# Kernel tuning notes

Measured on AMD Instinct MI355X. Metric: run time of the kernel, lower is better.

The kernel has to match this reference:

```python
import jax, jax.numpy as jnp
import numpy as np

N, E, B = 20000, 320000, 2
IN, HID, HEADS, OUT = 32, 64, 4, 8
N_MP = 2
SLOPE = 0.2  # GATConv default negative_slope


def setup_inputs() -> dict:
    key = jax.random.key(0)
    ks = jax.random.split(key, 10)
    s = 0.1
    return {
        "h": jax.random.normal(ks[0], (B, N, IN), jnp.float32),
        "edge_index": jax.random.randint(ks[1], (2, E), 0, N),
        "W_enc": jax.random.normal(ks[2], (IN, HID), jnp.float32) * s,
        "b_enc": jnp.zeros((HID,), jnp.float32),
        "W_gat": jax.random.normal(ks[3], (HID, HEADS * HID), jnp.float32) * s,
        "a_l": jax.random.normal(ks[4], (HEADS, HID), jnp.float32) * s,
        "a_r": jax.random.normal(ks[5], (HEADS, HID), jnp.float32) * s,
        "b_gat": jnp.zeros((HEADS * HID,), jnp.float32),
        "W_res": jax.random.normal(ks[6], (HID, HID), jnp.float32) * s,
        "b_res": jnp.zeros((HID,), jnp.float32),
        "W_dec": jax.random.normal(ks[7], (HID, OUT), jnp.float32) * s,
        "b_dec": jnp.zeros((OUT,), jnp.float32),
    }


def _gat(x, src, dst, W_gat, a_l, a_r, b_gat):
    # x: [N, B, HID] -> per-head projected features [N, B, HEADS, HID]
    ft = (x @ W_gat).reshape(N, B, HEADS, HID)
    el = jnp.einsum("nbhd,hd->nbh", ft, a_l)  # src attention term
    er = jnp.einsum("nbhd,hd->nbh", ft, a_r)  # dst attention term
    e = el[src] + er[dst]                      # [E, B, HEADS]
    e = jnp.where(e > 0, e, SLOPE * e)         # LeakyReLU
    # segment softmax over incoming edges of each dst node
    m = jax.ops.segment_max(e, dst, num_segments=N)
    e = jnp.exp(e - m[dst])
    z = jax.ops.segment_sum(e, dst, num_segments=N)
    alpha = e / z[dst]                         # [E, B, HEADS]
    msg = alpha[..., None] * ft[src]           # [E, B, HEADS, HID]
    agg = jax.ops.segment_sum(msg, dst, num_segments=N)
    return agg + b_gat.reshape(HEADS, HID)     # [N, B, HEADS, HID]


def reference(h, edge_index, W_enc, b_enc, W_gat, a_l, a_r, b_gat,
              W_res, b_res, W_dec, b_dec):
    src, dst = edge_index[0], edge_index[1]
    x = jnp.transpose(h, (1, 0, 2))            # [N, B, IN]
    x = x @ W_enc + b_enc                      # encoder (dropout in eval = identity)
    for _ in range(N_MP):
        gat_out = _gat(x, src, dst, W_gat, a_l, a_r, b_gat)
        x = jax.nn.elu(gat_out.mean(-2) + x @ W_res + b_res)
    x = x @ W_dec + b_dec
    return jnp.transpose(x, (1, 0, 2))         # [B, N, OUT]
```

## Files before the change

### kernel.cpp

```cpp
#include <hip/hip_runtime.h>
#include <hip/hip_bf16.h>

#define N_NODES 20000
#define N_EDGES 320000
#define BATCH 2
#define IN_DIM 32
#define HID 64
#define HEADS 4
#define OUT_DIM 8
#define ROWS (N_NODES * BATCH)
#define SLOPE 0.2f

typedef __hip_bfloat16 bf16;
typedef short v8s __attribute__((ext_vector_type(8)));
typedef float v4f __attribute__((ext_vector_type(4)));

#define WS_XA       0
#define WS_XB       1280000
#define WS_ELA      2560000
#define WS_ERA      2720000
#define WS_ELB      2880000
#define WS_ERB      3040000
#define WS_DEG      3200000
#define WS_ROWSTART 3220032
#define WS_CUR      3240064
#define WS_CSRC     3260096
#define WS_WGBPK    3580096
#define WS_WRESBPK  3588288
#define WS_WX8PK    3590336
#define WS_WENCBPK  3590848
#define WS_WDECBPK  3591872
#define WS_BGM      3592384
#define WS_END      3592448

__device__ __forceinline__ float us2f(unsigned short u) {
    union { unsigned int i; float f; } z; z.i = ((unsigned int)u) << 16; return z.f;
}
__device__ __forceinline__ unsigned short f2us(float f) {
    bf16 b = __float2bfloat16(f);
    return *(unsigned short*)&b;
}
__device__ __forceinline__ float ld(const void* p, int i, int isbf) {
    if (isbf) return us2f(((const unsigned short*)p)[i]);
    return ((const float*)p)[i];
}
__device__ __forceinline__ float lrexp(float v) {
    v = v > 0.f ? v : SLOPE * v;
    return __expf(fminf(v, 60.f));
}

__device__ __forceinline__ int sniff64(const void* h) {
    const unsigned short* u = (const unsigned short*)h;
    int lane = threadIdx.x & 63;
    unsigned short v = u[2 * lane];
    int ef = (v >> 7) & 0xFF;
    unsigned long long m = __ballot(ef >= 100 && ef <= 150);
    return __popcll(m) >= 48;
}

__global__ __launch_bounds__(256) void k_prep(const void* __restrict__ h,
                                              const void* __restrict__ Wg,
                                              const void* __restrict__ al,
                                              const void* __restrict__ ar,
                                              const void* __restrict__ Wr,
                                              const void* __restrict__ We,
                                              const void* __restrict__ Wd,
                                              const void* __restrict__ bg,
                                              unsigned short* __restrict__ WgBpk,
                                              unsigned short* __restrict__ WresBpk,
                                              unsigned short* __restrict__ Wx8pk,
                                              unsigned short* __restrict__ WencBpk,
                                              unsigned short* __restrict__ WdecBpk,
                                              float* __restrict__ bgm,
                                              int* __restrict__ deg) {
    int t = threadIdx.x, b = blockIdx.x;
    if (b >= 18) {
        int base = (b - 18) * 1024 + t * 4;
#pragma unroll
        for (int i = 0; i < 4; i++)
            if (base + i < 20032) deg[base + i] = 0;
        return;
    }
    const int isbf = sniff64(h);
    if (b < 16) {
#pragma unroll
        for (int q = 0; q < 4; q++) {
            int idx = b * 1024 + q * 256 + t;
            int j = idx & 7, m16 = (idx >> 3) & 15, quad = (idx >> 7) & 3;
            int ks = (idx >> 9) & 1, ct = (idx >> 10) & 3, hh = (idx >> 12) & 3;
            int k = ks * 32 + quad * 8 + j;
            int c = hh * 64 + ct * 16 + m16;
            WgBpk[idx] = f2us(ld(Wg, k * 256 + c, isbf));
        }
    } else if (b == 16) {
#pragma unroll
        for (int q = 0; q < 4; q++) {
            int idx = q * 256 + t;
            int j = idx & 7, m16 = (idx >> 3) & 15, quad = (idx >> 7) & 3;
            int ks = (idx >> 9) & 1;
            int k = ks * 32 + quad * 8 + j;
            float v = 0.f;
            if (m16 < 8) {
                int hh = m16 & 3, lr = m16 >> 2;
                const void* a = lr ? ar : al;
                for (int d = 0; d < 64; d++)
                    v += ld(Wg, k * 256 + hh * 64 + d, isbf) * ld(a, hh * 64 + d, isbf);
            }
            Wx8pk[idx] = f2us(v);
        }
#pragma unroll
        for (int q = 0; q < 8; q++) {
            int idx = q * 256 + t;
            int j = idx & 7, m16 = (idx >> 3) & 15, quad = (idx >> 7) & 3, ct = idx >> 9;
            int k = quad * 8 + j;
            WencBpk[idx] = f2us(ld(We, k * 64 + ct * 16 + m16, isbf));
        }
#pragma unroll
        for (int q = 0; q < 4; q++) {
            int idx = q * 256 + t;
            int j = idx & 7, m16 = (idx >> 3) & 15, quad = (idx >> 7) & 3;
            int ks = (idx >> 9) & 1;
            int k = ks * 32 + quad * 8 + j;
            WdecBpk[idx] = (m16 < 8) ? f2us(ld(Wd, k * 8 + m16, isbf)) : (unsigned short)0;
        }
        if (t < 64) {
            float s = 0.f;
            for (int hh = 0; hh < 4; hh++) s += ld(bg, hh * 64 + t, isbf);
            bgm[t] = 0.25f * s;
        }
    } else {
#pragma unroll
        for (int q = 0; q < 16; q++) {
            int idx = q * 256 + t;
            int j = idx & 7, m16 = (idx >> 3) & 15, quad = (idx >> 7) & 3;
            int ks = (idx >> 9) & 1;
            int k = ks * 32 + quad * 8 + j;
            WresBpk[idx] = f2us(ld(Wr, k * 64 + ((idx >> 10) & 3) * 16 + m16, isbf));
        }
    }
}

__global__ __launch_bounds__(256) void k_hist(const int* __restrict__ dst, int* __restrict__ deg) {
    int e = blockIdx.x * 256 + threadIdx.x;
    if (e < N_EDGES) atomicAdd(&deg[dst[e]], 1);
}

__global__ __launch_bounds__(1024) void k_scan(const int* __restrict__ deg,
                                               int* __restrict__ rowstart,
                                               int* __restrict__ cursor) {
    __shared__ int ssum[1024];
    int t = threadIdx.x;
    int base = t * 20;
    int local[20];
    int s = 0;
#pragma unroll
    for (int i = 0; i < 20; i++) {
        int v = (base + i < N_NODES) ? deg[base + i] : 0;
        local[i] = s;
        s += v;
    }
    ssum[t] = s;
    __syncthreads();
    for (int off = 1; off < 1024; off <<= 1) {
        int v = (t >= off) ? ssum[t - off] : 0;
        __syncthreads();
        if (t >= off) ssum[t] += v;
        __syncthreads();
    }
    int prev = (t == 0) ? 0 : ssum[t - 1];
#pragma unroll
    for (int i = 0; i < 20; i++) {
        if (base + i < N_NODES) {
            int v = prev + local[i];
            rowstart[base + i] = v;
            cursor[base + i] = v;
        }
    }
    if (t == 1023) rowstart[N_NODES] = ssum[1023];
}

__global__ __launch_bounds__(256) void k_scatter(const int* __restrict__ src,
                                                 const int* __restrict__ dst,
                                                 int* __restrict__ cursor,
                                                 int* __restrict__ csrc) {
    int e = blockIdx.x * 256 + threadIdx.x;
    if (e >= N_EDGES) return;
    int pos = atomicAdd(&cursor[dst[e]], 1);
    csrc[pos] = src[e];
}

__global__ __launch_bounds__(256) void k_enc2(const void* __restrict__ h,
                                              const unsigned short* __restrict__ WencBpk,
                                              const void* __restrict__ benc,
                                              const unsigned short* __restrict__ Wx8pk,
                                              unsigned int* __restrict__ xb32,
                                              float* __restrict__ el,
                                              float* __restrict__ er) {
    const int isbf = sniff64(h);
    __shared__ unsigned short sXb[64 * 64];
    int t = threadIdx.x;
    int w = t >> 6, lane = t & 63, quad = lane >> 4, m16 = lane & 15;
    int row0 = blockIdx.x * 64;
    int grow = row0 + w * 16 + m16;
    int n = grow >> 1, b = grow & 1;

    v8s Af;
    size_t hb = (size_t)(b * N_NODES + n) * IN_DIM + quad * 8;
    if (isbf) {
        Af = *(const v8s*)((const unsigned short*)h + hb);
    } else {
        const float4* hp = (const float4*)((const float*)h + hb);
        float4 xa = hp[0], xbv = hp[1];
        Af[0] = (short)f2us(xa.x);  Af[1] = (short)f2us(xa.y);
        Af[2] = (short)f2us(xa.z);  Af[3] = (short)f2us(xa.w);
        Af[4] = (short)f2us(xbv.x); Af[5] = (short)f2us(xbv.y);
        Af[6] = (short)f2us(xbv.z); Af[7] = (short)f2us(xbv.w);
    }

    v4f acc[4];
#pragma unroll
    for (int ct = 0; ct < 4; ct++) {
        v8s Bf = *(const v8s*)(WencBpk + ((ct << 9) | (quad << 7) | (m16 << 3)));
        acc[ct] = __builtin_amdgcn_mfma_f32_16x16x32_bf16(Af, Bf, (v4f)(0.f), 0, 0, 0);
    }

#pragma unroll
    for (int ct = 0; ct < 4; ct++) {
        int col = ct * 16 + m16;
        float bv = ld(benc, col, isbf);
        float vr[4];
        int rloc0 = w * 16 + quad * 4;
#pragma unroll
        for (int r = 0; r < 4; r++) {
            vr[r] = acc[ct][r] + bv;
            sXb[(rloc0 + r) * 64 + col] = f2us(vr[r]);
        }
        int nd0 = (row0 + rloc0) >> 1;
        xb32[(size_t)nd0 * 64 + col] =
            (unsigned int)f2us(vr[0]) | ((unsigned int)f2us(vr[1]) << 16);
        xb32[(size_t)(nd0 + 1) * 64 + col] =
            (unsigned int)f2us(vr[2]) | ((unsigned int)f2us(vr[3]) << 16);
    }
    __syncthreads();
    v4f e8 = (v4f)(0.f);
#pragma unroll
    for (int ks = 0; ks < 2; ks++) {
        v8s Af2 = *(const v8s*)(sXb + (w * 16 + m16) * 64 + ks * 32 + quad * 8);
        v8s Bf = *(const v8s*)(Wx8pk + (((ks * 4 + quad) << 7) + (m16 << 3)));
        e8 = __builtin_amdgcn_mfma_f32_16x16x32_bf16(Af2, Bf, e8, 0, 0, 0);
    }
    if (m16 < 8) {
#pragma unroll
        for (int r = 0; r < 4; r++) {
            int gr = row0 + w * 16 + quad * 4 + r;
            float v = e8[r];
            if (m16 < 4) el[gr * 4 + m16] = v;
            else         er[gr * 4 + (m16 - 4)] = v;
        }
    }
}

__global__ __launch_bounds__(256) void k_round(const int* __restrict__ rowstart,
                                               const int* __restrict__ csrc,
                                               const float* __restrict__ el_in,
                                               const float* __restrict__ er_in,
                                               const unsigned int* __restrict__ x_in,
                                               const unsigned short* __restrict__ WgBpk,
                                               const unsigned short* __restrict__ WresBpk,
                                               const unsigned short* __restrict__ Wx8pk,
                                               const unsigned short* __restrict__ WdecBpk,
                                               const void* __restrict__ h,
                                               const void* __restrict__ br,
                                               const void* __restrict__ bd,
                                               const float* __restrict__ bgm,
                                               unsigned int* __restrict__ x_out,
                                               float* __restrict__ el_out,
                                               float* __restrict__ er_out,
                                               void* __restrict__ out,
                                               int emit) {
    const int isbf = sniff64(h);
    __shared__ unsigned short sAgg[4 * 16 * 64];
    __shared__ unsigned short sXb[16 * 64];
    int t = threadIdx.x;
    int w = t >> 6, lane = t & 63, quad = lane >> 4, m16 = lane & 15;
    int i8 = m16 & 15 & 7;

    int nA = blockIdx.x * 8 + w * 2;
    int begA = rowstart[nA], endA = rowstart[nA + 1], endB = rowstart[nA + 2];
    int begB = endA;
    int rowNode = (m16 < 8) ? nA : (nA + 1);
    float erv = er_in[rowNode * 8 + i8];
    int beg = (quad < 2) ? begA : begB;
    int end = (quad < 2) ? endA : endB;
    int off = ((quad & 1) << 3);
    int active = ((m16 < 8) == (quad < 2));
    int itA = (endA - begA + 15) >> 4;
    int itB = (endB - begB + 15) >> 4;
    int itmax = itA > itB ? itA : itB;

    v4f accB0[4], accB1[4], accW;
#pragma unroll
    for (int tl = 0; tl < 4; tl++) { accB0[tl] = (v4f)(0.f); accB1[tl] = (v4f)(0.f); }
    accW = (v4f)(0.f);
    v8s Bones;
#pragma unroll
    for (int j = 0; j < 8; j++) Bones[j] = (short)0x3F80;

    for (int it = 0; it < itmax; ++it) {
        int p0 = beg + it * 16 + off;
        int s[8];
#pragma unroll
        for (int j = 0; j < 8; j++) {
            int idx = p0 + j;
            s[j] = csrc[idx < end ? idx : 0];
        }
        v8s Af;
#pragma unroll
        for (int j = 0; j < 8; j++) {
            float wv = 0.f;
            if (active && (p0 + j < end))
                wv = lrexp(el_in[s[j] * 8 + i8] + erv);
            Af[j] = (short)f2us(wv);
        }
        accW = __builtin_amdgcn_mfma_f32_16x16x32_bf16(Af, Bones, accW, 0, 0, 0);
#pragma unroll
        for (int tl = 0; tl < 4; tl++) {
            v8s B0, B1;
#pragma unroll
            for (int j = 0; j < 8; j++) {
                unsigned int q = x_in[(size_t)s[j] * 64 + tl * 16 + m16];
                B0[j] = (short)(q & 0xffffu);
                B1[j] = (short)(q >> 16);
            }
            accB0[tl] = __builtin_amdgcn_mfma_f32_16x16x32_bf16(Af, B0, accB0[tl], 0, 0, 0);
            accB1[tl] = __builtin_amdgcn_mfma_f32_16x16x32_bf16(Af, B1, accB1[tl], 0, 0, 0);
        }
    }

    {
        int row16 = w * 4 + quad;
        int swz = (row16 & 7) << 3;
#pragma unroll
        for (int tl = 0; tl < 4; tl++) {
#pragma unroll
            for (int r = 0; r < 4; r++) {
                float wss = accW[r];
                float mine = (quad & 1) ? accB1[tl][r] : accB0[tl][r];
                float v = (wss > 0.f) ? mine / (4.f * wss) : 0.f;
                int col = tl * 16 + m16;
                sAgg[((r * 16 + row16) << 6) | (col ^ swz)] = f2us(v);
            }
        }
    }
    __syncthreads();

    int grow0 = blockIdx.x * 16;
    int grow = grow0 + m16;
    int nd = grow >> 1;
    unsigned sh = (grow & 1) * 16;
    int ct = w;

    v4f acc = (v4f)(0.f);
#pragma unroll
    for (int hh = 0; hh < 4; hh++) {
#pragma unroll
        for (int ks = 0; ks < 2; ks++) {
            int si = ((hh * 16 + m16) << 6) | ((ks * 32 + quad * 8) ^ ((m16 & 7) << 3));
            v8s Af = *(const v8s*)(sAgg + si);
            v8s Bf = *(const v8s*)(WgBpk + ((hh << 12) | (ct << 10) | (ks << 9) | (quad << 7) | (m16 << 3)));
            acc = __builtin_amdgcn_mfma_f32_16x16x32_bf16(Af, Bf, acc, 0, 0, 0);
        }
    }
#pragma unroll
    for (int ks = 0; ks < 2; ks++) {
        const uint4* xp = (const uint4*)(x_in + (size_t)nd * 64 + ks * 32 + quad * 8);
        uint4 qa = xp[0], qb = xp[1];
        v8s Af;
        Af[0] = (short)((qa.x >> sh) & 0xffffu);
        Af[1] = (short)((qa.y >> sh) & 0xffffu);
        Af[2] = (short)((qa.z >> sh) & 0xffffu);
        Af[3] = (short)((qa.w >> sh) & 0xffffu);
        Af[4] = (short)((qb.x >> sh) & 0xffffu);
        Af[5] = (short)((qb.y >> sh) & 0xffffu);
        Af[6] = (short)((qb.z >> sh) & 0xffffu);
        Af[7] = (short)((qb.w >> sh) & 0xffffu);
        v8s Bf = *(const v8s*)(WresBpk + ((ct << 10) | (ks << 9) | (quad << 7) | (m16 << 3)));
        acc = __builtin_amdgcn_mfma_f32_16x16x32_bf16(Af, Bf, acc, 0, 0, 0);
    }

    {
        int col = ct * 16 + m16;
        float bv = ld(br, col, isbf) + bgm[col];
        float vr[4];
#pragma unroll
        for (int r = 0; r < 4; r++) {
            float v = acc[r] + bv;
            v = v > 0.f ? v : expm1f(v);
            vr[r] = v;
            sXb[(quad * 4 + r) * 64 + col] = f2us(v);
        }
        if (emit) {
            int nd0 = (grow0 + quad * 4) >> 1;
            x_out[(size_t)nd0 * 64 + col] =
                (unsigned int)f2us(vr[0]) | ((unsigned int)f2us(vr[1]) << 16);
            x_out[(size_t)(nd0 + 1) * 64 + col] =
                (unsigned int)f2us(vr[2]) | ((unsigned int)f2us(vr[3]) << 16);
        }
    }
    __syncthreads();

    if (w == 0) {
        if (emit) {
            v4f e8 = (v4f)(0.f);
#pragma unroll
            for (int ks = 0; ks < 2; ks++) {
                v8s Af = *(const v8s*)(sXb + m16 * 64 + ks * 32 + quad * 8);
                v8s Bf = *(const v8s*)(Wx8pk + (((ks * 4 + quad) << 7) + (m16 << 3)));
                e8 = __builtin_amdgcn_mfma_f32_16x16x32_bf16(Af, Bf, e8, 0, 0, 0);
            }
            if (m16 < 8) {
#pragma unroll
                for (int r = 0; r < 4; r++) {
                    int gr = grow0 + quad * 4 + r;
                    float v = e8[r];
                    if (m16 < 4) el_out[gr * 4 + m16] = v;
                    else         er_out[gr * 4 + (m16 - 4)] = v;
                }
            }
        } else {
            v4f o8 = (v4f)(0.f);
#pragma unroll
            for (int ks = 0; ks < 2; ks++) {
                v8s Af = *(const v8s*)(sXb + m16 * 64 + ks * 32 + quad * 8);
                v8s Bf = *(const v8s*)(WdecBpk + ((ks << 9) | (quad << 7) | (m16 << 3)));
                o8 = __builtin_amdgcn_mfma_f32_16x16x32_bf16(Af, Bf, o8, 0, 0, 0);
            }
            if (m16 < 8) {
                float bvd = ld(bd, m16, isbf);
#pragma unroll
                for (int r = 0; r < 4; r++) {
                    int gr = grow0 + quad * 4 + r;
                    int nn = gr >> 1, bb = gr & 1;
                    size_t oi = (size_t)(bb * N_NODES + nn) * OUT_DIM + m16;
                    float v = o8[r] + bvd;
                    if (isbf) ((unsigned short*)out)[oi] = f2us(v);
                    else      ((float*)out)[oi] = v;
                }
            }
        }
    }
}

extern "C" void kernel_launch(void* const* d_in, const int* in_sizes, int n_in,
                              void* d_out, int out_size, void* d_ws, size_t ws_size,
                              hipStream_t stream) {
    const void* h     = d_in[0];
    const int*  ei    = (const int*)d_in[1];
    const void* W_enc = d_in[2];
    const void* b_enc = d_in[3];
    const void* W_gat = d_in[4];
    const void* a_l   = d_in[5];
    const void* a_r   = d_in[6];
    const void* b_gat = d_in[7];
    const void* W_res = d_in[8];
    const void* b_res = d_in[9];
    const void* W_dec = d_in[10];
    const void* b_dec = d_in[11];

    float* ws = (float*)d_ws;
    unsigned int* xA = (unsigned int*)(ws + WS_XA);
    unsigned int* xB = (unsigned int*)(ws + WS_XB);
    float* elA      = ws + WS_ELA;
    float* erA      = ws + WS_ERA;
    float* elB      = ws + WS_ELB;
    float* erB      = ws + WS_ERB;
    int*   deg      = (int*)(ws + WS_DEG);
    int*   rowstart = (int*)(ws + WS_ROWSTART);
    int*   cursor   = (int*)(ws + WS_CUR);
    int*   csrc     = (int*)(ws + WS_CSRC);
    unsigned short* WgBpk   = (unsigned short*)(ws + WS_WGBPK);
    unsigned short* WresBpk = (unsigned short*)(ws + WS_WRESBPK);
    unsigned short* Wx8pk   = (unsigned short*)(ws + WS_WX8PK);
    unsigned short* WencBpk = (unsigned short*)(ws + WS_WENCBPK);
    unsigned short* WdecBpk = (unsigned short*)(ws + WS_WDECBPK);
    float* bgm      = ws + WS_BGM;

    const int* src = ei;
    const int* dst = ei + N_EDGES;

    k_prep<<<38, 256, 0, stream>>>(h, W_gat, a_l, a_r, W_res, W_enc, W_dec, b_gat,
                                   WgBpk, WresBpk, Wx8pk, WencBpk, WdecBpk, bgm, deg);
    k_hist<<<(N_EDGES + 255) / 256, 256, 0, stream>>>(dst, deg);
    k_scan<<<1, 1024, 0, stream>>>(deg, rowstart, cursor);
    k_scatter<<<(N_EDGES + 255) / 256, 256, 0, stream>>>(src, dst, cursor, csrc);

    k_enc2<<<ROWS / 64, 256, 0, stream>>>(h, WencBpk, b_enc, Wx8pk, xA, elA, erA);

    k_round<<<N_NODES / 8, 256, 0, stream>>>(rowstart, csrc, elA, erA, xA,
                                             WgBpk, WresBpk, Wx8pk, WdecBpk,
                                             h, b_res, b_dec, bgm,
                                             xB, elB, erB, d_out, 1);
    k_round<<<N_NODES / 8, 256, 0, stream>>>(rowstart, csrc, elB, erB, xB,
                                             WgBpk, WresBpk, Wx8pk, WdecBpk,
                                             h, b_res, b_dec, bgm,
                                             xA, elA, erA, d_out, 0);
}
```

Measured before the change: 238.6 us.

## Fuse prep, histogram and scan into one kernel; merge scatter with encoder

Replaces the separate prep, global-atomic histogram, single-block scan, scatter and encoder launches with two kernels. k_front has 18 blocks pack weights while 4 blocks each own a 5000-node destination range: each counts degrees in a shared-memory histogram, counts edges below its range for an offset, and scans locally. k_scatter_enc runs the CSR scatter and the encoder in one launch. This removes launch overhead and global atomics on the degree array, but each CSR block now reads all 320k dst indices.

```diff
diff --git a/kernel.cpp b/kernel.cpp
--- a/kernel.cpp
+++ b/kernel.cpp
@@ -21,7 +21,6 @@
 #define WS_ERA      2720000
 #define WS_ELB      2880000
 #define WS_ERB      3040000
-#define WS_DEG      3200000
 #define WS_ROWSTART 3220032
 #define WS_CUR      3240064
 #define WS_CSRC     3260096
@@ -58,30 +57,22 @@
     return __popcll(m) >= 48;
 }
 
-__global__ __launch_bounds__(256) void k_prep(const void* __restrict__ h,
-                                              const void* __restrict__ Wg,
-                                              const void* __restrict__ al,
-                                              const void* __restrict__ ar,
-                                              const void* __restrict__ Wr,
-                                              const void* __restrict__ We,
-                                              const void* __restrict__ Wd,
-                                              const void* __restrict__ bg,
-                                              unsigned short* __restrict__ WgBpk,
-                                              unsigned short* __restrict__ WresBpk,
-                                              unsigned short* __restrict__ Wx8pk,
-                                              unsigned short* __restrict__ WencBpk,
-                                              unsigned short* __restrict__ WdecBpk,
-                                              float* __restrict__ bgm,
-                                              int* __restrict__ deg) {
-    int t = threadIdx.x, b = blockIdx.x;
-    if (b >= 18) {
-        int base = (b - 18) * 1024 + t * 4;
-#pragma unroll
-        for (int i = 0; i < 4; i++)
-            if (base + i < 20032) deg[base + i] = 0;
-        return;
-    }
-    const int isbf = sniff64(h);
+
+__device__ __forceinline__ void prep_body(int b, int isbf,
+                                          const void* __restrict__ Wg,
+                                          const void* __restrict__ al,
+                                          const void* __restrict__ ar,
+                                          const void* __restrict__ Wr,
+                                          const void* __restrict__ We,
+                                          const void* __restrict__ Wd,
+                                          const void* __restrict__ bg,
+                                          unsigned short* __restrict__ WgBpk,
+                                          unsigned short* __restrict__ WresBpk,
+                                          unsigned short* __restrict__ Wx8pk,
+                                          unsigned short* __restrict__ WencBpk,
+                                          unsigned short* __restrict__ WdecBpk,
+                                          float* __restrict__ bgm) {
+    int t = threadIdx.x;
     if (b < 16) {
 #pragma unroll
         for (int q = 0; q < 4; q++) {
@@ -140,67 +131,18 @@
     }
 }
 
-__global__ __launch_bounds__(256) void k_hist(const int* __restrict__ dst, int* __restrict__ deg) {
-    int e = blockIdx.x * 256 + threadIdx.x;
-    if (e < N_EDGES) atomicAdd(&deg[dst[e]], 1);
-}
-
-__global__ __launch_bounds__(1024) void k_scan(const int* __restrict__ deg,
-                                               int* __restrict__ rowstart,
-                                               int* __restrict__ cursor) {
-    __shared__ int ssum[1024];
-    int t = threadIdx.x;
-    int base = t * 20;
-    int local[20];
-    int s = 0;
-#pragma unroll
-    for (int i = 0; i < 20; i++) {
-        int v = (base + i < N_NODES) ? deg[base + i] : 0;
-        local[i] = s;
-        s += v;
-    }
-    ssum[t] = s;
-    __syncthreads();
-    for (int off = 1; off < 1024; off <<= 1) {
-        int v = (t >= off) ? ssum[t - off] : 0;
-        __syncthreads();
-        if (t >= off) ssum[t] += v;
-        __syncthreads();
-    }
-    int prev = (t == 0) ? 0 : ssum[t - 1];
-#pragma unroll
-    for (int i = 0; i < 20; i++) {
-        if (base + i < N_NODES) {
-            int v = prev + local[i];
-            rowstart[base + i] = v;
-            cursor[base + i] = v;
-        }
-    }
-    if (t == 1023) rowstart[N_NODES] = ssum[1023];
-}
-
-__global__ __launch_bounds__(256) void k_scatter(const int* __restrict__ src,
-                                                 const int* __restrict__ dst,
-                                                 int* __restrict__ cursor,
-                                                 int* __restrict__ csrc) {
-    int e = blockIdx.x * 256 + threadIdx.x;
-    if (e >= N_EDGES) return;
-    int pos = atomicAdd(&cursor[dst[e]], 1);
-    csrc[pos] = src[e];
-}
-
-__global__ __launch_bounds__(256) void k_enc2(const void* __restrict__ h,
-                                              const unsigned short* __restrict__ WencBpk,
-                                              const void* __restrict__ benc,
-                                              const unsigned short* __restrict__ Wx8pk,
-                                              unsigned int* __restrict__ xb32,
-                                              float* __restrict__ el,
-                                              float* __restrict__ er) {
-    const int isbf = sniff64(h);
-    __shared__ unsigned short sXb[64 * 64];
+__device__ __forceinline__ void enc_unit(int u, int isbf,
+                                         const void* __restrict__ h,
+                                         const unsigned short* __restrict__ WencBpk,
+                                         const void* __restrict__ benc,
+                                         const unsigned short* __restrict__ Wx8pk,
+                                         unsigned int* __restrict__ xb32,
+                                         float* __restrict__ el,
+                                         float* __restrict__ er,
+                                         unsigned short* __restrict__ sXb) {
     int t = threadIdx.x;
     int w = t >> 6, lane = t & 63, quad = lane >> 4, m16 = lane & 15;
-    int row0 = blockIdx.x * 64;
+    int row0 = u * 64;
     int grow = row0 + w * 16 + m16;
     int n = grow >> 1, b = grow & 1;
 
@@ -258,6 +200,307 @@
             else         er[gr * 4 + (m16 - 4)] = v;
         }
     }
+}
+
+__device__ __forceinline__ void round_unit(int u, int isbf,
+                                           const int* __restrict__ rowstart,
+                                           const int* __restrict__ csrc,
+                                           const float* __restrict__ el_in,
+                                           const float* __restrict__ er_in,
+                                           const unsigned int* __restrict__ x_in,
+                                           const unsigned short* __restrict__ WgBpk,
+                                           const unsigned short* __restrict__ WresBpk,
+                                           const unsigned short* __restrict__ Wx8pk,
+                                           const unsigned short* __restrict__ WdecBpk,
+                                           const void* __restrict__ br,
+                                           const void* __restrict__ bd,
+                                           const float* __restrict__ bgm,
+                                           unsigned int* __restrict__ x_out,
+                                           float* __restrict__ el_out,
+                                           float* __restrict__ er_out,
+                                           void* __restrict__ out,
+                                           int emit,
+                                           unsigned short* __restrict__ sAgg,
+                                           unsigned short* __restrict__ sXb) {
+    int t = threadIdx.x;
+    int w = t >> 6, lane = t & 63, quad = lane >> 4, m16 = lane & 15;
+    int i8 = m16 & 7;
+
+    int nA = u * 8 + w * 2;
+    int begA = rowstart[nA], endA = rowstart[nA + 1], endB = rowstart[nA + 2];
+    int begB = endA;
+    int rowNode = (m16 < 8) ? nA : (nA + 1);
+    float erv = er_in[rowNode * 8 + i8];
+    int beg = (quad < 2) ? begA : begB;
+    int end = (quad < 2) ? endA : endB;
+    int off = ((quad & 1) << 3);
+    int active = ((m16 < 8) == (quad < 2));
+    int itA = (endA - begA + 15) >> 4;
+    int itB = (endB - begB + 15) >> 4;
+    int itmax = itA > itB ? itA : itB;
+
+    v4f accB0[4], accB1[4], accW;
+#pragma unroll
+    for (int tl = 0; tl < 4; tl++) { accB0[tl] = (v4f)(0.f); accB1[tl] = (v4f)(0.f); }
+    accW = (v4f)(0.f);
+    v8s Bones;
+#pragma unroll
+    for (int j = 0; j < 8; j++) Bones[j] = (short)0x3F80;
+
+    for (int it = 0; it < itmax; ++it) {
+        int p0 = beg + it * 16 + off;
+        int s[8];
+#pragma unroll
+        for (int j = 0; j < 8; j++) {
+            int idx = p0 + j;
+            s[j] = csrc[idx < end ? idx : 0];
+        }
+        v8s Af;
+#pragma unroll
+        for (int j = 0; j < 8; j++) {
+            float wv = 0.f;
+            if (active && (p0 + j < end))
+                wv = lrexp(el_in[s[j] * 8 + i8] + erv);
+            Af[j] = (short)f2us(wv);
+        }
+        accW = __builtin_amdgcn_mfma_f32_16x16x32_bf16(Af, Bones, accW, 0, 0, 0);
+#pragma unroll
+        for (int tl = 0; tl < 4; tl++) {
+            v8s B0, B1;
+#pragma unroll
+            for (int j = 0; j < 8; j++) {
+                unsigned int q = x_in[(size_t)s[j] * 64 + tl * 16 + m16];
+                B0[j] = (short)(q & 0xffffu);
+                B1[j] = (short)(q >> 16);
+            }
+            accB0[tl] = __builtin_amdgcn_mfma_f32_16x16x32_bf16(Af, B0, accB0[tl], 0, 0, 0);
+            accB1[tl] = __builtin_amdgcn_mfma_f32_16x16x32_bf16(Af, B1, accB1[tl], 0, 0, 0);
+        }
+    }
+
+    {
+        int row16 = w * 4 + quad;
+        int swz = (row16 & 7) << 3;
+#pragma unroll
+        for (int tl = 0; tl < 4; tl++) {
+#pragma unroll
+            for (int r = 0; r < 4; r++) {
+                float wss = accW[r];
+                float mine = (quad & 1) ? accB1[tl][r] : accB0[tl][r];
+                float v = (wss > 0.f) ? mine / (4.f * wss) : 0.f;
+                int col = tl * 16 + m16;
+                sAgg[((r * 16 + row16) << 6) | (col ^ swz)] = f2us(v);
+            }
+        }
+    }
+    __syncthreads();
+
+    int grow0 = u * 16;
+    int grow = grow0 + m16;
+    int nd = grow >> 1;
+    unsigned sh = (grow & 1) * 16;
+    int ct = w;
+
+    v4f acc = (v4f)(0.f);
+#pragma unroll
+    for (int hh = 0; hh < 4; hh++) {
+#pragma unroll
+        for (int ks = 0; ks < 2; ks++) {
+            int si = ((hh * 16 + m16) << 6) | ((ks * 32 + quad * 8) ^ ((m16 & 7) << 3));
+            v8s Af = *(const v8s*)(sAgg + si);
+            v8s Bf = *(const v8s*)(WgBpk + ((hh << 12) | (ct << 10) | (ks << 9) | (quad << 7) | (m16 << 3)));
+            acc = __builtin_amdgcn_mfma_f32_16x16x32_bf16(Af, Bf, acc, 0, 0, 0);
+        }
+    }
+#pragma unroll
+    for (int ks = 0; ks < 2; ks++) {
+        const uint4* xp = (const uint4*)(x_in + (size_t)nd * 64 + ks * 32 + quad * 8);
+        uint4 qa = xp[0], qb = xp[1];
+        v8s Af;
+        Af[0] = (short)((qa.x >> sh) & 0xffffu);
+        Af[1] = (short)((qa.y >> sh) & 0xffffu);
+        Af[2] = (short)((qa.z >> sh) & 0xffffu);
+        Af[3] = (short)((qa.w >> sh) & 0xffffu);
+        Af[4] = (short)((qb.x >> sh) & 0xffffu);
+        Af[5] = (short)((qb.y >> sh) & 0xffffu);
+        Af[6] = (short)((qb.z >> sh) & 0xffffu);
+        Af[7] = (short)((qb.w >> sh) & 0xffffu);
+        v8s Bf = *(const v8s*)(WresBpk + ((ct << 10) | (ks << 9) | (quad << 7) | (m16 << 3)));
+        acc = __builtin_amdgcn_mfma_f32_16x16x32_bf16(Af, Bf, acc, 0, 0, 0);
+    }
+
+    {
+        int col = ct * 16 + m16;
+        float bv = ld(br, col, isbf) + bgm[col];
+        float vr[4];
+#pragma unroll
+        for (int r = 0; r < 4; r++) {
+            float v = acc[r] + bv;
+            v = v > 0.f ? v : expm1f(v);
+            vr[r] = v;
+            sXb[(quad * 4 + r) * 64 + col] = f2us(v);
+        }
+        if (emit) {
+            int nd0 = (grow0 + quad * 4) >> 1;
+            x_out[(size_t)nd0 * 64 + col] =
+                (unsigned int)f2us(vr[0]) | ((unsigned int)f2us(vr[1]) << 16);
+            x_out[(size_t)(nd0 + 1) * 64 + col] =
+                (unsigned int)f2us(vr[2]) | ((unsigned int)f2us(vr[3]) << 16);
+        }
+    }
+    __syncthreads();
+
+    if (w == 0) {
+        if (emit) {
+            v4f e8 = (v4f)(0.f);
+#pragma unroll
+            for (int ks = 0; ks < 2; ks++) {
+                v8s Af = *(const v8s*)(sXb + m16 * 64 + ks * 32 + quad * 8);
+                v8s Bf = *(const v8s*)(Wx8pk + (((ks * 4 + quad) << 7) + (m16 << 3)));
+                e8 = __builtin_amdgcn_mfma_f32_16x16x32_bf16(Af, Bf, e8, 0, 0, 0);
+            }
+            if (m16 < 8) {
+#pragma unroll
+                for (int r = 0; r < 4; r++) {
+                    int gr = grow0 + quad * 4 + r;
+                    float v = e8[r];
+                    if (m16 < 4) el_out[gr * 4 + m16] = v;
+                    else         er_out[gr * 4 + (m16 - 4)] = v;
+                }
+            }
+        } else {
+            v4f o8 = (v4f)(0.f);
+#pragma unroll
+            for (int ks = 0; ks < 2; ks++) {
+                v8s Af = *(const v8s*)(sXb + m16 * 64 + ks * 32 + quad * 8);
+                v8s Bf = *(const v8s*)(WdecBpk + ((ks << 9) | (quad << 7) | (m16 << 3)));
+                o8 = __builtin_amdgcn_mfma_f32_16x16x32_bf16(Af, Bf, o8, 0, 0, 0);
+            }
+            if (m16 < 8) {
+                float bvd = ld(bd, m16, isbf);
+#pragma unroll
+                for (int r = 0; r < 4; r++) {
+                    int gr = grow0 + quad * 4 + r;
+                    int nn = gr >> 1, bb = gr & 1;
+                    size_t oi = (size_t)(bb * N_NODES + nn) * OUT_DIM + m16;
+                    float v = o8[r] + bvd;
+                    if (isbf) ((unsigned short*)out)[oi] = f2us(v);
+                    else      ((float*)out)[oi] = v;
+                }
+            }
+        }
+    }
+}
+
+__global__ __launch_bounds__(1024) void k_front(const void* __restrict__ h,
+                                                const int* __restrict__ ei,
+                                                const void* __restrict__ Wg,
+                                                const void* __restrict__ al,
+                                                const void* __restrict__ ar,
+                                                const void* __restrict__ Wr,
+                                                const void* __restrict__ We,
+                                                const void* __restrict__ Wd,
+                                                const void* __restrict__ bg,
+                                                unsigned short* __restrict__ WgBpk,
+                                                unsigned short* __restrict__ WresBpk,
+                                                unsigned short* __restrict__ Wx8pk,
+                                                unsigned short* __restrict__ WencBpk,
+                                                unsigned short* __restrict__ WdecBpk,
+                                                float* __restrict__ bgm,
+                                                int* __restrict__ rowstart,
+                                                int* __restrict__ cursor) {
+    int b = blockIdx.x, t = threadIdx.x;
+    if (b < 18) {
+        if (t < 256) {
+            const int isbf = sniff64(h);
+            prep_body(b, isbf, Wg, al, ar, Wr, We, Wd, bg,
+                      WgBpk, WresBpk, Wx8pk, WencBpk, WdecBpk, bgm);
+        }
+        return;
+    }
+    __shared__ unsigned int hist[2500];
+    __shared__ int ssum[1024];
+    const int* dstp = ei + N_EDGES;
+    int cb = b - 18;
+    int lo = cb * 5000, hi = lo + 5000;
+
+    for (int i = t; i < 2500; i += 1024) hist[i] = 0;
+    __syncthreads();
+
+    int below = 0;
+    for (int e = t; e < N_EDGES; e += 1024) {
+        int d = dstp[e];
+        below += (d < lo) ? 1 : 0;
+        if (d >= lo && d < hi) {
+            int ln = d - lo;
+            atomicAdd(&hist[ln >> 1], 1u << ((ln & 1) * 16));
+        }
+    }
+    ssum[t] = below;
+    __syncthreads();
+    for (int o = 512; o; o >>= 1) {
+        if (t < o) ssum[t] += ssum[t + o];
+        __syncthreads();
+    }
+    int base = ssum[0];
+    __syncthreads();
+
+    int nb = t * 5;
+    int loc[5];
+    int s = 0;
+#pragma unroll
+    for (int i = 0; i < 5; i++) {
+        int ln = nb + i;
+        int v = 0;
+        if (ln < 5000) {
+            unsigned q = hist[ln >> 1];
+            v = (ln & 1) ? (int)(q >> 16) : (int)(q & 0xffffu);
+        }
+        loc[i] = s;
+        s += v;
+    }
+    ssum[t] = s;
+    __syncthreads();
+    for (int o = 1; o < 1024; o <<= 1) {
+        int v = (t >= o) ? ssum[t - o] : 0;
+        __syncthreads();
+        if (t >= o) ssum[t] += v;
+        __syncthreads();
+    }
+    int prev = (t == 0) ? 0 : ssum[t - 1];
+#pragma unroll
+    for (int i = 0; i < 5; i++) {
+        int ln = nb + i;
+        if (ln < 5000) {
+            int v = base + prev + loc[i];
+            rowstart[lo + ln] = v;
+            cursor[lo + ln] = v;
+        }
+    }
+    if (cb == 3 && t == 1023) rowstart[N_NODES] = base + ssum[1023];
+}
+
+__global__ __launch_bounds__(256) void k_scatter_enc(const int* __restrict__ src,
+                                                     const int* __restrict__ dst,
+                                                     int* __restrict__ cursor,
+                                                     int* __restrict__ csrc,
+                                                     const void* __restrict__ h,
+                                                     const unsigned short* __restrict__ WencBpk,
+                                                     const void* __restrict__ benc,
+                                                     const unsigned short* __restrict__ Wx8pk,
+                                                     unsigned int* __restrict__ xb32,
+                                                     float* __restrict__ el,
+                                                     float* __restrict__ er) {
+    int b = blockIdx.x;
+    if (b < N_EDGES / 256) {
+        int e = b * 256 + threadIdx.x;
+        int pos = atomicAdd(&cursor[dst[e]], 1);
+        csrc[pos] = src[e];
+        return;
+    }
+    const int isbf = sniff64(h);
+    __shared__ unsigned short sXb[64 * 64];
+    enc_unit(b - N_EDGES / 256, isbf, h, WencBpk, benc, Wx8pk, xb32, el, er, sXb);
 }
 
 __global__ __launch_bounds__(256) void k_round(const int* __restrict__ rowstart,
@@ -279,176 +522,10 @@
                                                void* __restrict__ out,
                                                int emit) {
     const int isbf = sniff64(h);
-    __shared__ unsigned short sAgg[4 * 16 * 64];
-    __shared__ unsigned short sXb[16 * 64];
-    int t = threadIdx.x;
-    int w = t >> 6, lane = t & 63, quad = lane >> 4, m16 = lane & 15;
-    int i8 = m16 & 15 & 7;
-
-    int nA = blockIdx.x * 8 + w * 2;
-    int begA = rowstart[nA], endA = rowstart[nA + 1], endB = rowstart[nA + 2];
-    int begB = endA;
-    int rowNode = (m16 < 8) ? nA : (nA + 1);
-    float erv = er_in[rowNode * 8 + i8];
-    int beg = (quad < 2) ? begA : begB;
-    int end = (quad < 2) ? endA : endB;
-    int off = ((quad & 1) << 3);
-    int active = ((m16 < 8) == (quad < 2));
-    int itA = (endA - begA + 15) >> 4;
-    int itB = (endB - begB + 15) >> 4;
-    int itmax = itA > itB ? itA : itB;
-
-    v4f accB0[4], accB1[4], accW;
-#pragma unroll
-    for (int tl = 0; tl < 4; tl++) { accB0[tl] = (v4f)(0.f); accB1[tl] = (v4f)(0.f); }
-    accW = (v4f)(0.f);
-    v8s Bones;
-#pragma unroll
-    for (int j = 0; j < 8; j++) Bones[j] = (short)0x3F80;
-
-    for (int it = 0; it < itmax; ++it) {
-        int p0 = beg + it * 16 + off;
-        int s[8];
-#pragma unroll
-        for (int j = 0; j < 8; j++) {
-            int idx = p0 + j;
-            s[j] = csrc[idx < end ? idx : 0];
-        }
-        v8s Af;
-#pragma unroll
-        for (int j = 0; j < 8; j++) {
-            float wv = 0.f;
-            if (active && (p0 + j < end))
-                wv = lrexp(el_in[s[j] * 8 + i8] + erv);
-            Af[j] = (short)f2us(wv);
-        }
-        accW = __builtin_amdgcn_mfma_f32_16x16x32_bf16(Af, Bones, accW, 0, 0, 0);
-#pragma unroll
-        for (int tl = 0; tl < 4; tl++) {
-            v8s B0, B1;
-#pragma unroll
-            for (int j = 0; j < 8; j++) {
-                unsigned int q = x_in[(size_t)s[j] * 64 + tl * 16 + m16];
-                B0[j] = (short)(q & 0xffffu);
-                B1[j] = (short)(q >> 16);
-            }
-            accB0[tl] = __builtin_amdgcn_mfma_f32_16x16x32_bf16(Af, B0, accB0[tl], 0, 0, 0);
-            accB1[tl] = __builtin_amdgcn_mfma_f32_16x16x32_bf16(Af, B1, accB1[tl], 0, 0, 0);
-        }
-    }
-
-    {
-        int row16 = w * 4 + quad;
-        int swz = (row16 & 7) << 3;
-#pragma unroll
-        for (int tl = 0; tl < 4; tl++) {
-#pragma unroll
-            for (int r = 0; r < 4; r++) {
-                float wss = accW[r];
-                float mine = (quad & 1) ? accB1[tl][r] : accB0[tl][r];
-                float v = (wss > 0.f) ? mine / (4.f * wss) : 0.f;
-                int col = tl * 16 + m16;
-                sAgg[((r * 16 + row16) << 6) | (col ^ swz)] = f2us(v);
-            }
-        }
-    }
-    __syncthreads();
-
-    int grow0 = blockIdx.x * 16;
-    int grow = grow0 + m16;
-    int nd = grow >> 1;
-    unsigned sh = (grow & 1) * 16;
-    int ct = w;
-
-    v4f acc = (v4f)(0.f);
-#pragma unroll
-    for (int hh = 0; hh < 4; hh++) {
-#pragma unroll
-        for (int ks = 0; ks < 2; ks++) {
-            int si = ((hh * 16 + m16) << 6) | ((ks * 32 + quad * 8) ^ ((m16 & 7) << 3));
-            v8s Af = *(const v8s*)(sAgg + si);
-            v8s Bf = *(const v8s*)(WgBpk + ((hh << 12) | (ct << 10) | (ks << 9) | (quad << 7) | (m16 << 3)));
-            acc = __builtin_amdgcn_mfma_f32_16x16x32_bf16(Af, Bf, acc, 0, 0, 0);
-        }
-    }
-#pragma unroll
-    for (int ks = 0; ks < 2; ks++) {
-        const uint4* xp = (const uint4*)(x_in + (size_t)nd * 64 + ks * 32 + quad * 8);
-        uint4 qa = xp[0], qb = xp[1];
-        v8s Af;
-        Af[0] = (short)((qa.x >> sh) & 0xffffu);
-        Af[1] = (short)((qa.y >> sh) & 0xffffu);
-        Af[2] = (short)((qa.z >> sh) & 0xffffu);
-        Af[3] = (short)((qa.w >> sh) & 0xffffu);
-        Af[4] = (short)((qb.x >> sh) & 0xffffu);
-        Af[5] = (short)((qb.y >> sh) & 0xffffu);
-        Af[6] = (short)((qb.z >> sh) & 0xffffu);
-        Af[7] = (short)((qb.w >> sh) & 0xffffu);
-        v8s Bf = *(const v8s*)(WresBpk + ((ct << 10) | (ks << 9) | (quad << 7) | (m16 << 3)));
-        acc = __builtin_amdgcn_mfma_f32_16x16x32_bf16(Af, Bf, acc, 0, 0, 0);
-    }
-
-    {
-        int col = ct * 16 + m16;
-        float bv = ld(br, col, isbf) + bgm[col];
-        float vr[4];
-#pragma unroll
-        for (int r = 0; r < 4; r++) {
-            float v = acc[r] + bv;
-            v = v > 0.f ? v : expm1f(v);
-            vr[r] = v;
-            sXb[(quad * 4 + r) * 64 + col] = f2us(v);
-        }
-        if (emit) {
-            int nd0 = (grow0 + quad * 4) >> 1;
-            x_out[(size_t)nd0 * 64 + col] =
-                (unsigned int)f2us(vr[0]) | ((unsigned int)f2us(vr[1]) << 16);
-            x_out[(size_t)(nd0 + 1) * 64 + col] =
-                (unsigned int)f2us(vr[2]) | ((unsigned int)f2us(vr[3]) << 16);
-        }
-    }
-    __syncthreads();
-
-    if (w == 0) {
-        if (emit) {
-            v4f e8 = (v4f)(0.f);
-#pragma unroll
-            for (int ks = 0; ks < 2; ks++) {
-                v8s Af = *(const v8s*)(sXb + m16 * 64 + ks * 32 + quad * 8);
-                v8s Bf = *(const v8s*)(Wx8pk + (((ks * 4 + quad) << 7) + (m16 << 3)));
-                e8 = __builtin_amdgcn_mfma_f32_16x16x32_bf16(Af, Bf, e8, 0, 0, 0);
-            }
-            if (m16 < 8) {
-#pragma unroll
-                for (int r = 0; r < 4; r++) {
-                    int gr = grow0 + quad * 4 + r;
-                    float v = e8[r];
-                    if (m16 < 4) el_out[gr * 4 + m16] = v;
-                    else         er_out[gr * 4 + (m16 - 4)] = v;
-                }
-            }
-        } else {
-            v4f o8 = (v4f)(0.f);
-#pragma unroll
-            for (int ks = 0; ks < 2; ks++) {
-                v8s Af = *(const v8s*)(sXb + m16 * 64 + ks * 32 + quad * 8);
-                v8s Bf = *(const v8s*)(WdecBpk + ((ks << 9) | (quad << 7) | (m16 << 3)));
-                o8 = __builtin_amdgcn_mfma_f32_16x16x32_bf16(Af, Bf, o8, 0, 0, 0);
-            }
-            if (m16 < 8) {
-                float bvd = ld(bd, m16, isbf);
-#pragma unroll
-                for (int r = 0; r < 4; r++) {
-                    int gr = grow0 + quad * 4 + r;
-                    int nn = gr >> 1, bb = gr & 1;
-                    size_t oi = (size_t)(bb * N_NODES + nn) * OUT_DIM + m16;
-                    float v = o8[r] + bvd;
-                    if (isbf) ((unsigned short*)out)[oi] = f2us(v);
-                    else      ((float*)out)[oi] = v;
-                }
-            }
-        }
-    }
+    __shared__ unsigned short smem[5120];
+    round_unit(blockIdx.x, isbf, rowstart, csrc, el_in, er_in, x_in,
+               WgBpk, WresBpk, Wx8pk, WdecBpk, br, bd, bgm,
+               x_out, el_out, er_out, out, emit, smem, smem + 4096);
 }
 
 extern "C" void kernel_launch(void* const* d_in, const int* in_sizes, int n_in,
@@ -474,7 +551,6 @@
     float* erA      = ws + WS_ERA;
     float* elB      = ws + WS_ELB;
     float* erB      = ws + WS_ERB;
-    int*   deg      = (int*)(ws + WS_DEG);
     int*   rowstart = (int*)(ws + WS_ROWSTART);
     int*   cursor   = (int*)(ws + WS_CUR);
     int*   csrc     = (int*)(ws + WS_CSRC);
@@ -488,14 +564,12 @@
     const int* src = ei;
     const int* dst = ei + N_EDGES;
 
-    k_prep<<<38, 256, 0, stream>>>(h, W_gat, a_l, a_r, W_res, W_enc, W_dec, b_gat,
-                                   WgBpk, WresBpk, Wx8pk, WencBpk, WdecBpk, bgm, deg);
-    k_hist<<<(N_EDGES + 255) / 256, 256, 0, stream>>>(dst, deg);
-    k_scan<<<1, 1024, 0, stream>>>(deg, rowstart, cursor);
-    k_scatter<<<(N_EDGES + 255) / 256, 256, 0, stream>>>(src, dst, cursor, csrc);
-
-    k_enc2<<<ROWS / 64, 256, 0, stream>>>(h, WencBpk, b_enc, Wx8pk, xA, elA, erA);
-
+    k_front<<<22, 1024, 0, stream>>>(h, ei, W_gat, a_l, a_r, W_res, W_enc, W_dec, b_gat,
+                                     WgBpk, WresBpk, Wx8pk, WencBpk, WdecBpk, bgm,
+                                     rowstart, cursor);
+    k_scatter_enc<<<N_EDGES / 256 + ROWS / 64, 256, 0, stream>>>(src, dst, cursor, csrc,
+                                                                 h, WencBpk, b_enc, Wx8pk,
+                                                                 xA, elA, erA);
     k_round<<<N_NODES / 8, 256, 0, stream>>>(rowstart, csrc, elA, erA, xA,
                                              WgBpk, WresBpk, Wx8pk, WdecBpk,
                                              h, b_res, b_dec, bgm,
```

Measured after the change: 288.3 us. +20.8%, slower.
